# Kernel optimization log

Measured on AMD Instinct MI355X. Metric: run time of the kernel, lower is better.

The kernel has to match this reference:

```python
import jax, jax.numpy as jnp
import numpy as np

B, K, D, H = 16384, 3, 1024, 16
DH = D // H  # head_dim = 64


def setup_inputs() -> dict:
    key = jax.random.key(0)
    ks = jax.random.split(key, 12)
    s = 1.0 / np.sqrt(D)
    inp = {
        "tokens": jax.random.normal(ks[0], (B, K, D), dtype=jnp.float32),
        "ctx": jax.random.normal(ks[1], (B, 1, D), dtype=jnp.float32),
        "Wq": jax.random.uniform(ks[2], (D, D), jnp.float32, -s, s),
        "bq": jnp.zeros((D,), jnp.float32),
        "Wk": jax.random.uniform(ks[3], (D, D), jnp.float32, -s, s),
        "bk": jnp.zeros((D,), jnp.float32),
        "Wv": jax.random.uniform(ks[4], (D, D), jnp.float32, -s, s),
        "bv": jnp.zeros((D,), jnp.float32),
        "Wc": jax.random.uniform(ks[5], (D, D), jnp.float32, -s, s),
        "bc": jnp.zeros((D,), jnp.float32),
        "Wo": jax.random.uniform(ks[6], (D, D), jnp.float32, -s, s),
        "bo": jnp.zeros((D,), jnp.float32),
    }
    return inp


def _split_heads(x):
    # (B, L, D) -> (B, H, L, DH)
    Bq, L, _ = x.shape
    return x.reshape(Bq, L, H, DH).transpose(0, 2, 1, 3)


def reference(tokens, ctx, Wq, bq, Wk, bk, Wv, bv, Wc, bc, Wo, bo):
    q = _split_heads(tokens @ Wq.T + bq)          # (B,H,K,DH)
    k = _split_heads(tokens @ Wk.T + bk)          # (B,H,K,DH)
    v = _split_heads(tokens @ Wv.T + bv)          # (B,H,K,DH)
    c = _split_heads(ctx @ Wc.T + bc)             # (B,H,1,DH)
    k_ctx = k * c                                  # context-modulated keys
    v_ctx = v * c                                  # context-modulated values
    scores = jnp.einsum("bhqd,bhkd->bhqk", q, k_ctx) / jnp.sqrt(jnp.float32(DH))
    probs = jax.nn.softmax(scores, axis=-1)       # dropout p=0.0 -> identity
    out = jnp.einsum("bhqk,bhkd->bhqd", probs, v_ctx)
    out = out.transpose(0, 2, 1, 3).reshape(tokens.shape[0], K, D)  # merge heads
    return out @ Wo.T + bo
```

## Files before the change

kernel.cpp:

```cpp
#include <hip/hip_runtime.h>
#include <hip/hip_bf16.h>

#define BB 16384
#define KK 3
#define DD 1024
#define HH 16

typedef __attribute__((ext_vector_type(8))) short bf16x8;
typedef __attribute__((ext_vector_type(4))) float f32x4;
typedef unsigned int u32;

__device__ __forceinline__ void load_lds16(const void* g, void* l) {
  __builtin_amdgcn_global_load_lds(
      (const __attribute__((address_space(1))) u32*)g,
      (__attribute__((address_space(3))) u32*)l,
      16, 0, 0);
}

__device__ __forceinline__ unsigned short f2bf(float f) {
  __hip_bfloat16 h = __float2bfloat16(f);
  unsigned short u;
  __builtin_memcpy(&u, &h, 2);
  return u;
}

__device__ __forceinline__ float bf2f(unsigned short u) {
  union { float f; u32 i; } cv;
  cv.i = ((u32)u) << 16;
  return cv.f;
}

__global__ void cast_f32_bf16(const float* __restrict__ in,
                              unsigned short* __restrict__ out, int n4) {
  int stride = gridDim.x * blockDim.x;
  for (int i = blockIdx.x * blockDim.x + threadIdx.x; i < n4; i += stride) {
    float4 v = ((const float4*)in)[i];
    ushort4 o;
    o.x = f2bf(v.x);
    o.y = f2bf(v.y);
    o.z = f2bf(v.z);
    o.w = f2bf(v.w);
    ((ushort4*)out)[i] = o;
  }
}

template <bool OUT_F32>
__global__ __launch_bounds__(512, 2)
void gemm256(const __hip_bfloat16* __restrict__ A,
             const __hip_bfloat16* __restrict__ Bt,
             const float* __restrict__ bias,
             void* __restrict__ Cout,
             int M, int N, int K) {
  __shared__ __align__(128) char lds[131072];

  const int nTn = N >> 8;
  const int nwg = (M >> 8) * nTn;
  int bid = blockIdx.x;
  bid = (bid & 7) * (nwg >> 3) + (bid >> 3);
  const int tm = bid / nTn;
  const int tn = bid % nTn;

  const int tid = threadIdx.x;
  const int l = tid & 63;
  const int w = tid >> 6;
  const int wm = w >> 2;
  const int wn = w & 3;
  const int l15 = l & 15;
  const int g = l >> 4;
  const int l7 = l15 & 7;

  const int aBase = (l15 << 7) + (((wm << 2) + g) ^ l7) * 16;
  const int bBase = 16384 + ((((wn & 1) << 6) + l15) << 7) +
                    ((((wn >> 1) << 2) + g) ^ l7) * 16;

  const size_t strideK = (size_t)K * 2;
  const char* Ab = (const char*)A + (size_t)tm * 256 * strideK;
  const char* Bb = (const char*)Bt + (size_t)tn * 256 * strideK;
  const int q = (tid & 7) ^ ((tid >> 3) & 7);
  const size_t g0 = (size_t)((q >> 2) * 128 + (tid >> 3)) * strideK + (q & 3) * 16;
  const size_t g1 = g0 + (size_t)64 * strideK;
  const int sld = tid << 4;

  f32x4 acc[8][4] = {};
  const int nkt = K >> 5;

#define STAGE_AB(T)                                                       \
  {                                                                       \
    char* sb = lds + (((T) & 3) << 15);                                   \
    const char* ga = Ab + ((size_t)(T) << 6);                             \
    const char* gb = Bb + ((size_t)(T) << 6);                             \
    load_lds16(ga + g0, sb + sld);                                        \
    load_lds16(ga + g1, sb + 8192 + sld);                                 \
    load_lds16(gb + g0, sb + 16384 + sld);                                \
    load_lds16(gb + g1, sb + 24576 + sld);                                \
  }

  STAGE_AB(0);
  STAGE_AB(1);
  STAGE_AB(2);

  for (int kt = 0; kt < nkt; ++kt) {
    if (kt <= nkt - 3)
      asm volatile("s_waitcnt vmcnt(8)" ::: "memory");
    else if (kt == nkt - 2)
      asm volatile("s_waitcnt vmcnt(4)" ::: "memory");
    else
      asm volatile("s_waitcnt vmcnt(0)" ::: "memory");
    __builtin_amdgcn_s_barrier();
    asm volatile("" ::: "memory");

    const char* slot = lds + ((kt & 3) << 15);
    bf16x8 bfr[4], af[8];
#pragma unroll
    for (int n = 0; n < 4; ++n)
      bfr[n] = *(const bf16x8*)(slot + bBase + (n << 11));
#pragma unroll
    for (int m = 0; m < 8; ++m)
      af[m] = *(const bf16x8*)(slot + aBase + (m << 11));

    if (kt + 3 < nkt) STAGE_AB(kt + 3);

    __builtin_amdgcn_s_setprio(1);
#pragma unroll
    for (int m = 0; m < 8; ++m)
#pragma unroll
      for (int n = 0; n < 4; ++n)
        acc[m][n] = __builtin_amdgcn_mfma_f32_16x16x32_bf16(af[m], bfr[n],
                                                            acc[m][n], 0, 0, 0);
    __builtin_amdgcn_s_setprio(0);
  }
#undef STAGE_AB

  const int cbase = tn * 256 + (wn << 6) + l15;
  float b4[4];
#pragma unroll
  for (int n = 0; n < 4; ++n) b4[n] = bias[cbase + (n << 4)];
  const size_t rbase = (size_t)tm * 256 + (wm << 7) + ((l >> 4) << 2);
#pragma unroll
  for (int m = 0; m < 8; ++m) {
#pragma unroll
    for (int j = 0; j < 4; ++j) {
      const size_t row = rbase + (m << 4) + j;
#pragma unroll
      for (int n = 0; n < 4; ++n) {
        const int col = cbase + (n << 4);
        float v = acc[m][n][j] + b4[n];
        if (OUT_F32)
          ((float*)Cout)[row * N + col] = v;
        else
          ((unsigned short*)Cout)[row * N + col] = f2bf(v);
      }
    }
  }
}

__global__ __launch_bounds__(256)
void attn_kernel(const unsigned short* __restrict__ QKV,
                 const unsigned short* __restrict__ Cp,
                 unsigned short* __restrict__ Out) {
  const int t = threadIdx.x;
  const int grp = (blockIdx.x << 4) + (t >> 4);
  const int x = t & 15;
  const int b = grp >> 4;
  const int h = grp & 15;

  const size_t col = (size_t)h * 64 + (x << 2);
  const size_t qbase = (size_t)b * 3 * 3072 + col;

  ushort4 cu = *(const ushort4*)&Cp[(size_t)b * 1024 + col];
  float c[4] = {bf2f(cu.x), bf2f(cu.y), bf2f(cu.z), bf2f(cu.w)};

  float q[3][4], kc[3][4], vc[3][4];
#pragma unroll
  for (int i = 0; i < 3; ++i) {
    ushort4 qu = *(const ushort4*)&QKV[qbase + (size_t)i * 3072];
    ushort4 ku = *(const ushort4*)&QKV[qbase + (size_t)i * 3072 + 1024];
    ushort4 vu = *(const ushort4*)&QKV[qbase + (size_t)i * 3072 + 2048];
    q[i][0] = bf2f(qu.x); q[i][1] = bf2f(qu.y); q[i][2] = bf2f(qu.z); q[i][3] = bf2f(qu.w);
    kc[i][0] = bf2f(ku.x) * c[0]; kc[i][1] = bf2f(ku.y) * c[1];
    kc[i][2] = bf2f(ku.z) * c[2]; kc[i][3] = bf2f(ku.w) * c[3];
    vc[i][0] = bf2f(vu.x) * c[0]; vc[i][1] = bf2f(vu.y) * c[1];
    vc[i][2] = bf2f(vu.z) * c[2]; vc[i][3] = bf2f(vu.w) * c[3];
  }

  float s[9];
#pragma unroll
  for (int i = 0; i < 3; ++i)
#pragma unroll
    for (int j = 0; j < 3; ++j)
      s[i * 3 + j] = q[i][0] * kc[j][0] + q[i][1] * kc[j][1] +
                     q[i][2] * kc[j][2] + q[i][3] * kc[j][3];

#pragma unroll
  for (int off = 8; off > 0; off >>= 1)
#pragma unroll
    for (int e = 0; e < 9; ++e)
      s[e] += __shfl_xor(s[e], off, 64);

  const float scale = 0.125f;
#pragma unroll
  for (int i = 0; i < 3; ++i) {
    float s0 = s[i * 3 + 0] * scale;
    float s1 = s[i * 3 + 1] * scale;
    float s2 = s[i * 3 + 2] * scale;
    float m = fmaxf(fmaxf(s0, s1), s2);
    float p0 = expf(s0 - m), p1 = expf(s1 - m), p2 = expf(s2 - m);
    float inv = 1.0f / (p0 + p1 + p2);
    ushort4 o;
    o.x = f2bf((p0 * vc[0][0] + p1 * vc[1][0] + p2 * vc[2][0]) * inv);
    o.y = f2bf((p0 * vc[0][1] + p1 * vc[1][1] + p2 * vc[2][1]) * inv);
    o.z = f2bf((p0 * vc[0][2] + p1 * vc[1][2] + p2 * vc[2][2]) * inv);
    o.w = f2bf((p0 * vc[0][3] + p1 * vc[1][3] + p2 * vc[2][3]) * inv);
    *(ushort4*)&Out[(size_t)(b * 3 + i) * 1024 + col] = o;
  }
}

extern "C" void kernel_launch(void* const* d_in, const int* in_sizes, int n_in,
                              void* d_out, int out_size, void* d_ws, size_t ws_size,
                              hipStream_t stream) {
  const float* tokens = (const float*)d_in[0];
  const float* ctx    = (const float*)d_in[1];
  const float* Wq     = (const float*)d_in[2];
  const float* bq     = (const float*)d_in[3];
  const float* Wk     = (const float*)d_in[4];
  const float* bk     = (const float*)d_in[5];
  const float* Wv     = (const float*)d_in[6];
  const float* bv     = (const float*)d_in[7];
  const float* Wc     = (const float*)d_in[8];
  const float* bc     = (const float*)d_in[9];
  const float* Wo     = (const float*)d_in[10];
  const float* bo     = (const float*)d_in[11];

  const int M  = BB * KK;
  const int Mc = BB;
  const int D  = DD;

  char* p = (char*)d_ws;
  auto carve = [&](size_t bytes) {
    char* r = p;
    p += (bytes + 255) & ~(size_t)255;
    return r;
  };
  unsigned short* Xb   = (unsigned short*)carve((size_t)M * D * 2);
  unsigned short* Cin  = (unsigned short*)carve((size_t)Mc * D * 2);
  unsigned short* Wqkv = (unsigned short*)carve((size_t)3 * D * D * 2);
  unsigned short* Wcb  = (unsigned short*)carve((size_t)D * D * 2);
  unsigned short* Wob  = (unsigned short*)carve((size_t)D * D * 2);
  float*          bqkv = (float*)carve((size_t)3 * D * 4);
  unsigned short* QKV  = (unsigned short*)carve((size_t)M * 3 * D * 2);
  unsigned short* Cpr  = (unsigned short*)carve((size_t)Mc * D * 2);

  hipLaunchKernelGGL(cast_f32_bf16, dim3(4096), dim3(256), 0, stream, tokens, Xb, M * D / 4);
  hipLaunchKernelGGL(cast_f32_bf16, dim3(2048), dim3(256), 0, stream, ctx, Cin, Mc * D / 4);
  hipLaunchKernelGGL(cast_f32_bf16, dim3(512), dim3(256), 0, stream, Wq, Wqkv, D * D / 4);
  hipLaunchKernelGGL(cast_f32_bf16, dim3(512), dim3(256), 0, stream, Wk, Wqkv + D * D, D * D / 4);
  hipLaunchKernelGGL(cast_f32_bf16, dim3(512), dim3(256), 0, stream, Wv, Wqkv + 2 * D * D, D * D / 4);
  hipLaunchKernelGGL(cast_f32_bf16, dim3(512), dim3(256), 0, stream, Wc, Wcb, D * D / 4);
  hipLaunchKernelGGL(cast_f32_bf16, dim3(512), dim3(256), 0, stream, Wo, Wob, D * D / 4);
  hipMemcpyAsync(bqkv, bq, D * 4, hipMemcpyDeviceToDevice, stream);
  hipMemcpyAsync(bqkv + D, bk, D * 4, hipMemcpyDeviceToDevice, stream);
  hipMemcpyAsync(bqkv + 2 * D, bv, D * 4, hipMemcpyDeviceToDevice, stream);

  hipLaunchKernelGGL((gemm256<false>), dim3((M / 256) * (3 * D / 256)), dim3(512), 0, stream,
                     (const __hip_bfloat16*)Xb, (const __hip_bfloat16*)Wqkv, bqkv,
                     (void*)QKV, M, 3 * D, D);
  hipLaunchKernelGGL((gemm256<false>), dim3((Mc / 256) * (D / 256)), dim3(512), 0, stream,
                     (const __hip_bfloat16*)Cin, (const __hip_bfloat16*)Wcb, bc,
                     (void*)Cpr, Mc, D, D);
  hipLaunchKernelGGL(attn_kernel, dim3(BB * HH / 16), dim3(256), 0, stream, QKV, Cpr, Xb);
  hipLaunchKernelGGL((gemm256<true>), dim3((M / 256) * (D / 256)), dim3(512), 0, stream,
                     (const __hip_bfloat16*)Xb, (const __hip_bfloat16*)Wob, bo,
                     d_out, M, D, D);
}
```

Before: 656.5 us.

## Restructure GEMM main loop into double-buffered 64-wide K tiles with quadrant MFMA interleave

The bf16 GEMM main loop changes from a 4-slot ring of K=32 tiles to two 64KB LDS buffers holding K=64 tiles. Each buffer is processed as four MFMA quadrants, with LDS reads and global-to-LDS staging of later tile halves placed between barrier-separated MFMA phases. The aim is to overlap memory traffic with compute at a finer grain and to raise arithmetic per barrier. In exchange there are many more barriers per iteration and higher register pressure from the 16+8 fragment arrays, and the loop assumes K is a multiple of 128.

Measured after the change: 628.1 us. 4.3% less time.

```diff
diff --git a/kernel.cpp b/kernel.cpp
--- a/kernel.cpp
+++ b/kernel.cpp
@@ -69,67 +69,107 @@
   const int g = l >> 4;
   const int l7 = l15 & 7;
 
-  const int aBase = (l15 << 7) + (((wm << 2) + g) ^ l7) * 16;
-  const int bBase = 16384 + ((((wn & 1) << 6) + l15) << 7) +
-                    ((((wn >> 1) << 2) + g) ^ l7) * 16;
+  const int cs0 = ((g ^ l7) << 4);
+  const int cs1 = (((4 | g) ^ l7) << 4);
+  const int aRowB = ((wm << 7) + l15) << 7;
+  const int bColB = 32768 + (((wn << 6) + l15) << 7);
 
   const size_t strideK = (size_t)K * 2;
   const char* Ab = (const char*)A + (size_t)tm * 256 * strideK;
   const char* Bb = (const char*)Bt + (size_t)tn * 256 * strideK;
-  const int q = (tid & 7) ^ ((tid >> 3) & 7);
-  const size_t g0 = (size_t)((q >> 2) * 128 + (tid >> 3)) * strideK + (q & 3) * 16;
-  const size_t g1 = g0 + (size_t)64 * strideK;
-  const int sld = tid << 4;
+  const size_t sOff = (size_t)(tid >> 3) * strideK +
+                      (size_t)(((tid & 7) ^ ((tid >> 3) & 7)) << 4);
+  const int sldst = tid << 4;
+
+  char* const sl0 = lds;
+  char* const sl1 = lds + 65536;
 
   f32x4 acc[8][4] = {};
-  const int nkt = K >> 5;
-
-#define STAGE_AB(T)                                                       \
-  {                                                                       \
-    char* sb = lds + (((T) & 3) << 15);                                   \
-    const char* ga = Ab + ((size_t)(T) << 6);                             \
-    const char* gb = Bb + ((size_t)(T) << 6);                             \
-    load_lds16(ga + g0, sb + sld);                                        \
-    load_lds16(ga + g1, sb + 8192 + sld);                                 \
-    load_lds16(gb + g0, sb + 16384 + sld);                                \
-    load_lds16(gb + g1, sb + 24576 + sld);                                \
-  }
-
-  STAGE_AB(0);
-  STAGE_AB(1);
-  STAGE_AB(2);
-
-  for (int kt = 0; kt < nkt; ++kt) {
-    if (kt <= nkt - 3)
-      asm volatile("s_waitcnt vmcnt(8)" ::: "memory");
-    else if (kt == nkt - 2)
-      asm volatile("s_waitcnt vmcnt(4)" ::: "memory");
-    else
-      asm volatile("s_waitcnt vmcnt(0)" ::: "memory");
-    __builtin_amdgcn_s_barrier();
-    asm volatile("" ::: "memory");
-
-    const char* slot = lds + ((kt & 3) << 15);
-    bf16x8 bfr[4], af[8];
-#pragma unroll
-    for (int n = 0; n < 4; ++n)
-      bfr[n] = *(const bf16x8*)(slot + bBase + (n << 11));
-#pragma unroll
-    for (int m = 0; m < 8; ++m)
-      af[m] = *(const bf16x8*)(slot + aBase + (m << 11));
-
-    if (kt + 3 < nkt) STAGE_AB(kt + 3);
-
-    __builtin_amdgcn_s_setprio(1);
-#pragma unroll
-    for (int m = 0; m < 8; ++m)
-#pragma unroll
-      for (int n = 0; n < 4; ++n)
-        acc[m][n] = __builtin_amdgcn_mfma_f32_16x16x32_bf16(af[m], bfr[n],
-                                                            acc[m][n], 0, 0, 0);
-    __builtin_amdgcn_s_setprio(0);
-  }
-#undef STAGE_AB
+  bf16x8 aF[16], bF[8];
+  const int njt = K >> 7;
+
+#define STG_A(T, H)                                                        \
+  {                                                                        \
+    char* d = lds + (((T) & 1) << 16) + ((H) << 14) + sldst;               \
+    const char* s = Ab + ((size_t)(T) << 7) +                              \
+                    ((size_t)((H) << 7)) * strideK + sOff;                 \
+    load_lds16(s, d);                                                      \
+    load_lds16(s + 64 * strideK, d + 8192);                                \
+  }
+#define STG_B(T, H)                                                        \
+  {                                                                        \
+    char* d = lds + (((T) & 1) << 16) + 32768 + ((H) << 14) + sldst;       \
+    const char* s = Bb + ((size_t)(T) << 7) +                              \
+                    ((size_t)((H) << 7)) * strideK + sOff;                 \
+    load_lds16(s, d);                                                      \
+    load_lds16(s + 64 * strideK, d + 8192);                                \
+  }
+#define RD_A2(SB, m)                                                       \
+  aF[2 * (m)] = *(const bf16x8*)((SB) + aRowB + ((m) << 11) + cs0);        \
+  aF[2 * (m) + 1] = *(const bf16x8*)((SB) + aRowB + ((m) << 11) + cs1);
+#define RD_B2(SB, n)                                                       \
+  bF[2 * (n)] = *(const bf16x8*)((SB) + bColB + ((n) << 11) + cs0);        \
+  bF[2 * (n) + 1] = *(const bf16x8*)((SB) + bColB + ((n) << 11) + cs1);
+#define MFMA_Q(MH, NH)                                                     \
+  __builtin_amdgcn_s_setprio(1);                                           \
+  _Pragma("unroll") for (int mm = 0; mm < 4; ++mm)                         \
+      _Pragma("unroll") for (int nn = 0; nn < 2; ++nn)                     \
+          _Pragma("unroll") for (int kh = 0; kh < 2; ++kh)                 \
+              acc[(MH)*4 + mm][(NH)*2 + nn] =                              \
+                  __builtin_amdgcn_mfma_f32_16x16x32_bf16(                 \
+                      aF[2 * ((MH)*4 + mm) + kh],                          \
+                      bF[2 * ((NH)*2 + nn) + kh],                          \
+                      acc[(MH)*4 + mm][(NH)*2 + nn], 0, 0, 0);             \
+  __builtin_amdgcn_s_setprio(0);
+#define BAR  __builtin_amdgcn_s_barrier(); asm volatile("" ::: "memory");
+#define LGKM0 asm volatile("s_waitcnt lgkmcnt(0)" ::: "memory");
+
+  STG_A(0, 0); STG_A(0, 1); STG_B(0, 0); STG_B(0, 1);
+  STG_A(1, 0); STG_A(1, 1);
+  asm volatile("s_waitcnt vmcnt(4)" ::: "memory");
+  BAR
+
+  for (int j = 0; j < njt; ++j) {
+    const int t1 = 2 * j + 1, t2 = 2 * j + 2, t3 = 2 * j + 3;
+    const bool full = (j < njt - 1);
+
+    RD_B2(sl0, 0) RD_B2(sl0, 1)
+    RD_A2(sl0, 0) RD_A2(sl0, 1) RD_A2(sl0, 2) RD_A2(sl0, 3)
+    STG_B(t1, 0)
+    BAR LGKM0 MFMA_Q(0, 0) BAR
+    RD_A2(sl0, 4) RD_A2(sl0, 5) RD_A2(sl0, 6) RD_A2(sl0, 7)
+    STG_B(t1, 1)
+    BAR LGKM0 MFMA_Q(1, 0) BAR
+    RD_B2(sl0, 2) RD_B2(sl0, 3)
+    if (full) STG_A(t2, 0)
+    BAR LGKM0 MFMA_Q(0, 1) BAR
+    if (full) STG_A(t2, 1)
+    if (full) { asm volatile("s_waitcnt vmcnt(4)" ::: "memory"); }
+    else      { asm volatile("s_waitcnt vmcnt(0)" ::: "memory"); }
+    BAR MFMA_Q(1, 1) BAR
+
+    RD_B2(sl1, 0) RD_B2(sl1, 1)
+    RD_A2(sl1, 0) RD_A2(sl1, 1) RD_A2(sl1, 2) RD_A2(sl1, 3)
+    if (full) STG_B(t2, 0)
+    BAR LGKM0 MFMA_Q(0, 0) BAR
+    RD_A2(sl1, 4) RD_A2(sl1, 5) RD_A2(sl1, 6) RD_A2(sl1, 7)
+    if (full) STG_B(t2, 1)
+    BAR LGKM0 MFMA_Q(1, 0) BAR
+    RD_B2(sl1, 2) RD_B2(sl1, 3)
+    if (full) STG_A(t3, 0)
+    BAR LGKM0 MFMA_Q(0, 1) BAR
+    if (full) STG_A(t3, 1)
+    if (full) { asm volatile("s_waitcnt vmcnt(4)" ::: "memory"); }
+    else      { asm volatile("s_waitcnt vmcnt(0)" ::: "memory"); }
+    BAR MFMA_Q(1, 1) BAR
+  }
+#undef STG_A
+#undef STG_B
+#undef RD_A2
+#undef RD_B2
+#undef MFMA_Q
+#undef BAR
+#undef LGKM0
 
   const int cbase = tn * 256 + (wn << 6) + l15;
   float b4[4];
```
